# Optimization experiments

Measured on AMD Instinct MI355X. Metric: run time of the kernel, lower is better.

The kernel has to match this reference:

```python
import jax, jax.numpy as jnp
import numpy as np

B, S, D_IN, D_Q, D_V, H = 2, 2048, 1024, 1024, 1024, 16
HD_Q, HD_V = D_Q // H, D_V // H
SCALE = float(D_Q) ** 0.5  # source scales by sqrt(d_q), NOT sqrt(head_dim)


def setup_inputs() -> dict:
    key = jax.random.key(0)
    k1, k2, k3, k4, k5 = jax.random.split(key, 5)
    return {
        "x": jax.random.normal(k1, (B, S, D_IN), dtype=jnp.float32),
        "w_q": jax.random.normal(k2, (D_IN, D_Q), dtype=jnp.float32),
        "w_k": jax.random.normal(k3, (D_IN, D_Q), dtype=jnp.float32),
        "w_v": jax.random.normal(k4, (D_IN, D_V), dtype=jnp.float32),
        "W_o": jax.random.normal(k5, (D_IN, D_V), dtype=jnp.float32),
    }


def reference(x, w_q, w_k, w_v, W_o):
    b, s, _ = x.shape
    # projections: [b, s, d]
    q = x @ w_q
    k = x @ w_k
    v = x @ w_v
    # split heads -> [b, h, s, hd]
    Q = q.reshape(b, s, H, HD_Q).transpose(0, 2, 1, 3)
    K = k.reshape(b, s, H, HD_Q).transpose(0, 2, 1, 3)
    V = v.reshape(b, s, H, HD_V).transpose(0, 2, 1, 3)
    # full [b, h, s, s] score matrix (naive attention, as in source)
    scores = jnp.einsum("bhqd,bhkd->bhqk", Q, K)
    # FAITHFUL QUIRK: source applies softmax over dim=0 (batch axis)
    attn = jax.nn.softmax(scores / SCALE, axis=0)
    vals = jnp.einsum("bhqk,bhkd->bhqd", attn, V)
    vals = vals.transpose(0, 2, 1, 3).reshape(b, s, D_V)
    return vals @ W_o
```

## Files before the change

### kernel.cpp

```cpp
#include <hip/hip_runtime.h>


typedef _Float16 f16;
typedef __attribute__((ext_vector_type(8))) _Float16 f16x8;
typedef __attribute__((ext_vector_type(4))) _Float16 f16x4;
typedef __attribute__((ext_vector_type(4))) float f32x4;
typedef __attribute__((ext_vector_type(16))) float f32x16;

#define MFMA16(a,b,c)  __builtin_amdgcn_mfma_f32_16x16x32_f16(a,b,c,0,0,0)
#define MFMA32(a,b,c)  __builtin_amdgcn_mfma_f32_32x32x16_f16(a,b,c,0,0,0)
#define GLD16(gp, lp) __builtin_amdgcn_global_load_lds(                         \
    (const __attribute__((address_space(1))) void*)(gp),                        \
    (__attribute__((address_space(3))) void*)(lp), 16, 0, 0)

__global__ __launch_bounds__(256) void prep(const float* __restrict__ x,
                                            const float* __restrict__ w0, const float* __restrict__ w1,
                                            const float* __restrict__ w2, const float* __restrict__ w3,
                                            f16* __restrict__ xh,
                                            f16* __restrict__ o0, f16* __restrict__ o1,
                                            f16* __restrict__ o2, f16* __restrict__ o3) {
    const int bb = blockIdx.x;
    const int tid = threadIdx.x;
    if (bb >= 1024) {
        int i = (bb - 1024) * 256 + tid;
        float4 v = ((const float4*)x)[i];
        f16x4 h;
        h[0] = (f16)v.x; h[1] = (f16)v.y; h[2] = (f16)v.z; h[3] = (f16)v.w;
        *(f16x4*)(xh + (long)i * 4) = h;
        return;
    }
    const float* w; f16* o;
    switch (bb & 3) {
        case 0: w = w0; o = o0; break;
        case 1: w = w1; o = o1; break;
        case 2: w = w2; o = o2; break;
        default: w = w3; o = o3; break;
    }
    __shared__ alignas(16) f16 t[64][72];
    const int d0 = ((bb >> 2) & 15) * 64, j0 = (bb >> 6) * 64;
    #pragma unroll
    for (int it = 0; it < 4; ++it) {
        int idx = it * 256 + tid;
        int row = idx >> 4, c4 = idx & 15;
        float4 v = *(const float4*)(w + (long)(d0 + row) * 1024 + j0 + c4 * 4);
        f16x4 h;
        h[0] = (f16)v.x; h[1] = (f16)v.y; h[2] = (f16)v.z; h[3] = (f16)v.w;
        *(f16x4*)&t[row][c4 * 4] = h;
    }
    __syncthreads();
    #pragma unroll
    for (int it = 0; it < 4; ++it) {
        int idx = it * 256 + tid;
        int jr = idx >> 4, d4 = idx & 15;
        f16x4 h;
        #pragma unroll
        for (int m = 0; m < 4; ++m) h[m] = t[d4 * 4 + m][jr];
        *(f16x4*)(o + (long)(j0 + jr) * 1024 + d0 + d4 * 4) = h;
    }
}

__global__ __launch_bounds__(256, 1) void gemm_qkv(const f16* __restrict__ A,
                                                   const f16* __restrict__ Wt,
                                                   f16* __restrict__ Qg,
                                                   f16* __restrict__ Kg,
                                                   f16* __restrict__ Vtg) {
    __shared__ alignas(16) f16 smem[16384];
    f16* As = smem;
    f16* Bs = smem + 8192;
    const int tid = threadIdx.x;
    const int wave = tid >> 6, lane = tid & 63;
    const int l15 = lane & 15, lq = lane >> 4;
    const int sw = l15 & 7;
    const int m0 = blockIdx.x * 128, n0 = blockIdx.y * 128;
    const int wr = (wave >> 1) * 64, wc = (wave & 1) * 64;
    const int r8 = lane >> 3;
    const int swc8 = ((lane & 7) ^ r8) * 8;

    f32x4 acc[4][4] = {};

    for (int kt = 0; kt < 16; ++kt) {
        __syncthreads();
        #pragma unroll
        for (int i = 0; i < 4; ++i) {
            GLD16(A  + (long)(m0 + wave * 32 + i * 8 + r8) * 1024 + kt * 64 + swc8, As + (wave * 32 + i * 8) * 64);
            GLD16(Wt + (long)(n0 + wave * 32 + i * 8 + r8) * 1024 + kt * 64 + swc8, Bs + (wave * 32 + i * 8) * 64);
        }
        __syncthreads();
        #pragma unroll
        for (int s2 = 0; s2 < 2; ++s2) {
            const int rc = ((s2 * 4 + lq) ^ sw) << 3;
            f16x8 af[4], bf[4];
            #pragma unroll
            for (int i = 0; i < 4; ++i) af[i] = *(const f16x8*)&As[(wr + i * 16 + l15) * 64 + rc];
            #pragma unroll
            for (int j = 0; j < 4; ++j) bf[j] = *(const f16x8*)&Bs[(wc + j * 16 + l15) * 64 + rc];
            #pragma unroll
            for (int i = 0; i < 4; ++i)
                #pragma unroll
                for (int j = 0; j < 4; ++j)
                    acc[i][j] = MFMA16(af[i], bf[j], acc[i][j]);
        }
    }

    const int sel = n0 >> 10;
    const int nb = n0 - (sel << 10);

    if (sel < 2) {
        f16* dst = sel == 0 ? Qg : Kg;
        const float qs = sel == 0 ? 0.045084219f : 1.0f;
        __syncthreads();
        #pragma unroll
        for (int i = 0; i < 4; ++i)
            #pragma unroll
            for (int j = 0; j < 4; ++j) {
                int row0 = wr + i * 16 + lq * 4;
                int colb = wc + j * 16 + l15;
                int chunk = colb >> 3, sub = colb & 7;
                #pragma unroll
                for (int r = 0; r < 4; ++r) {
                    int row = row0 + r;
                    smem[row * 128 + ((chunk ^ (row & 7)) << 3) + sub] = (f16)(acc[i][j][r] * qs);
                }
            }
        __syncthreads();
        #pragma unroll
        for (int e = 0; e < 8; ++e) {
            int id = e * 256 + tid;
            int row = id >> 4, c = id & 15;
            f16x8 v = *(const f16x8*)&smem[row * 128 + ((c ^ (row & 7)) << 3)];
            int gr = m0 + row, b = gr >> 11, s = gr & 2047;
            int gc = nb + c * 8, hh = gc >> 6, hd = gc & 63;
            *(f16x8*)(dst + (long)((b * 16 + hh) * 2048 + s) * 64 + hd) = v;
        }
    } else {
        #pragma unroll
        for (int i = 0; i < 4; ++i)
            #pragma unroll
            for (int j = 0; j < 4; ++j) {
                int gr0 = m0 + wr + i * 16 + lq * 4;
                int gc  = nb + wc + j * 16 + l15;
                int b = gr0 >> 11, s = gr0 & 2047;
                int hh = gc >> 6, hd = gc & 63;
                f16x4 v;
                #pragma unroll
                for (int r = 0; r < 4; ++r) v[r] = (f16)acc[i][j][r];
                *(f16x4*)(Vtg + (long)((b * 16 + hh) * 64 + hd) * 2048 + s) = v;
            }
    }
}

template<int NSUM>
__global__ __launch_bounds__(256, 1) void gemm_out(const f16* __restrict__ A0,
                                                   const f16* __restrict__ A1,
                                                   const f16* __restrict__ A2,
                                                   const f16* __restrict__ A3,
                                                   const f16* __restrict__ Bt,
                                                   float* __restrict__ outp) {
    __shared__ alignas(16) f16 As[64][72];
    __shared__ alignas(16) f16 Bs[128][64];
    const int tid = threadIdx.x;
    const int wave = tid >> 6, lane = tid & 63;
    const int l15 = lane & 15, lq = lane >> 4;
    const int sw = l15 & 7;
    const int m0 = blockIdx.x * 64, n0 = blockIdx.y * 128;
    const int wr = (wave >> 1) * 32, wc = (wave & 1) * 64;
    const int r8 = lane >> 3;
    const int swc8 = ((lane & 7) ^ r8) * 8;

    f32x4 acc[2][4] = {};

    for (int kt = 0; kt < 16; ++kt) {
        __syncthreads();
        #pragma unroll
        for (int it = 0; it < 2; ++it) {
            int idx = it * 256 + tid;
            int row = idx >> 3, c = idx & 7;
            long off = (long)(m0 + row) * 1024 + kt * 64 + c * 8;
            f16x8 a = *(const f16x8*)(A0 + off) + *(const f16x8*)(A1 + off);
            if constexpr (NSUM >= 3) a = a + *(const f16x8*)(A2 + off);
            if constexpr (NSUM >= 4) a = a + *(const f16x8*)(A3 + off);
            *(f16x8*)&As[row][c * 8] = a;
        }
        #pragma unroll
        for (int i = 0; i < 4; ++i)
            GLD16(Bt + (long)(n0 + wave * 32 + i * 8 + r8) * 1024 + kt * 64 + swc8, &Bs[wave * 32 + i * 8][0]);
        __syncthreads();
        #pragma unroll
        for (int s2 = 0; s2 < 2; ++s2) {
            const int rc = ((s2 * 4 + lq) ^ sw) << 3;
            f16x8 af[2], bf[4];
            #pragma unroll
            for (int i = 0; i < 2; ++i) af[i] = *(const f16x8*)&As[wr + i * 16 + l15][s2 * 32 + lq * 8];
            #pragma unroll
            for (int j = 0; j < 4; ++j) bf[j] = *(const f16x8*)&Bs[wc + j * 16 + l15][rc];
            #pragma unroll
            for (int i = 0; i < 2; ++i)
                #pragma unroll
                for (int j = 0; j < 4; ++j)
                    acc[i][j] = MFMA16(af[i], bf[j], acc[i][j]);
        }
    }

    #pragma unroll
    for (int i = 0; i < 2; ++i)
        #pragma unroll
        for (int j = 0; j < 4; ++j) {
            int gr0 = m0 + wr + i * 16 + lq * 4;
            int gc  = n0 + wc + j * 16 + l15;
            #pragma unroll
            for (int r = 0; r < 4; ++r)
                outp[(long)(gr0 + r) * 1024 + gc] = acc[i][j][r];
        }
}

__global__ __launch_bounds__(256, 3) void attention_kernel(const f16* __restrict__ Qg,
                                                           const f16* __restrict__ Kg,
                                                           const f16* __restrict__ Vtg,
                                                           f16* __restrict__ v0,
                                                           f16* __restrict__ v1,
                                                           f16* __restrict__ v2) {
    __shared__ alignas(16) f16 Ks [3][2][32][64];
    __shared__ alignas(16) f16 Vts[3][2][64][32];
    const int tid = threadIdx.x;
    const int wave = tid >> 6, lane = tid & 63;
    const int l31 = lane & 31, hi = lane >> 5;
    const int kchunk = l31 & 7;
    const int vcb = (l31 >> 1) & 3;

    const int NS = gridDim.x >> 8;
    const int bid = blockIdx.x;
    const int xcd = bid & 7, sl = bid >> 3;
    const int h  = xcd * 2 + (sl & 1);
    const int qt = (sl >> 1) & 15, ks = sl >> 5;
    const int q0 = qt * 128;
    const int kb = 64 / NS, krem = 64 % NS;
    const int nt = kb + (ks < krem ? 1 : 0);
    const int ts0 = ks * kb + (ks < krem ? ks : krem);
    const int key0 = ts0 * 32;
    f16* vals = ks == 0 ? v0 : ks == 1 ? v1 : v2;
    const int qr = q0 + wave * 32;

    f16x8 qfr[2][4];
    #pragma unroll
    for (int b2 = 0; b2 < 2; ++b2)
        #pragma unroll
        for (int s2 = 0; s2 < 4; ++s2)
            qfr[b2][s2] = *(const f16x8*)(Qg + (long)((b2 * 16 + h) * 2048 + qr + l31) * 64
                                          + s2 * 16 + hi * 8);

    f32x16 acc[2][2] = {};

    const int tb = wave & 1;
    const int r8 = lane >> 3;
    const int swc8 = ((lane & 7) ^ r8) * 8;
    const f16* kbase = Kg  + (long)((tb * 16 + h) * 2048 + key0) * 64 + r8 * 64 + swc8;
    const f16* vbase = Vtg + (long)((tb * 16 + h) * 64 + (lane >> 2)) * 2048 + key0
                       + ((lane & 3) ^ ((lane >> 3) & 3)) * 8;

    auto stage = [&](int kt, int buf) {
        if (wave < 2) {
            const f16* g = kbase + kt * 2048;
            f16* l = &Ks[buf][tb][0][0];
            #pragma unroll
            for (int i = 0; i < 4; ++i) GLD16(g + i * 512, l + i * 512);
        } else {
            const f16* g = vbase + kt * 32;
            f16* l = &Vts[buf][tb][0][0];
            #pragma unroll
            for (int i = 0; i < 4; ++i) GLD16(g + (long)i * 16 * 2048, l + i * 512);
        }
    };

    const f16* VtsF = &Vts[0][0][0][0];
    const f16x8 ones8 = {(f16)1.f,(f16)1.f,(f16)1.f,(f16)1.f,(f16)1.f,(f16)1.f,(f16)1.f,(f16)1.f};

    stage(0, 0);
    stage(1, 1);
    int cur = 0, nx2 = 2;
    for (int kt = 0; kt < nt; ++kt) {
        if (kt == nt - 1) asm volatile("s_waitcnt vmcnt(0)" ::: "memory");
        else              asm volatile("s_waitcnt vmcnt(4)" ::: "memory");
        __builtin_amdgcn_s_barrier();
        __builtin_amdgcn_sched_barrier(0);
        if (kt + 2 < nt) stage(kt + 2, nx2);

        f32x16 S0 = {}, S1 = {};
        __builtin_amdgcn_s_setprio(1);
        #pragma unroll
        for (int s2 = 0; s2 < 4; ++s2) {
            const int rc = ((s2 * 2 + hi) ^ kchunk) << 3;
            f16x8 a0 = *(const f16x8*)&Ks[cur][0][l31][rc];
            f16x8 a1 = *(const f16x8*)&Ks[cur][1][l31][rc];
            S0 = MFMA32(a0, qfr[0][s2], S0);
            S1 = MFMA32(a1, qfr[1][s2], S1);
        }
        __builtin_amdgcn_s_setprio(0);

        unsigned pk[8];
        #pragma unroll
        for (int p = 0; p < 8; ++p) {
            float e0 = __builtin_amdgcn_exp2f(S1[2 * p]     - S0[2 * p]);
            float e1 = __builtin_amdgcn_exp2f(S1[2 * p + 1] - S0[2 * p + 1]);
            float pa = __builtin_amdgcn_rcpf(1.0f + e0);
            float pb = __builtin_amdgcn_rcpf(1.0f + e1);
            auto h2 = __builtin_amdgcn_cvt_pkrtz(pa, pb);
            pk[p] = __builtin_bit_cast(unsigned, h2);
        }

        f16x8 pf0[2], pf1[2];
        #pragma unroll
        for (int keyh = 0; keyh < 2; ++keyh) {
            unsigned a0 = pk[4 * keyh + 0], b0 = pk[4 * keyh + 2];
            unsigned a1 = pk[4 * keyh + 1], b1 = pk[4 * keyh + 3];
            asm("v_permlane32_swap_b32 %0, %1" : "+v"(a0), "+v"(b0));
            asm("v_permlane32_swap_b32 %0, %1" : "+v"(a1), "+v"(b1));
            union { unsigned u[4]; f16x8 v; } m;
            m.u[0] = a0; m.u[1] = a1; m.u[2] = b0; m.u[3] = b1;
            pf0[keyh] = m.v;
            pf1[keyh] = ones8 - m.v;
        }

        __builtin_amdgcn_s_setprio(1);
        #pragma unroll
        for (int pb = 0; pb < 2; ++pb)
            #pragma unroll
            for (int keyh = 0; keyh < 2; ++keyh) {
                const f16x8 pfr = pb ? pf1[keyh] : pf0[keyh];
                #pragma unroll
                for (int hdh = 0; hdh < 2; ++hdh) {
                    f16x8 vf = *(const f16x8*)&VtsF[cur * 4096 + pb * 2048 + hdh * 1024
                                                    + l31 * 32 + (((keyh * 2 + hi) ^ vcb) << 3)];
                    acc[pb][hdh] = MFMA32(vf, pfr, acc[pb][hdh]);
                }
            }
        __builtin_amdgcn_s_setprio(0);

        cur = cur == 2 ? 0 : cur + 1;
        nx2 = nx2 == 2 ? 0 : nx2 + 1;
    }

    #pragma unroll
    for (int pb = 0; pb < 2; ++pb)
        #pragma unroll
        for (int hdh = 0; hdh < 2; ++hdh)
            #pragma unroll
            for (int g = 0; g < 4; ++g) {
                f16x4 ov;
                #pragma unroll
                for (int r2 = 0; r2 < 4; ++r2) ov[r2] = (f16)acc[pb][hdh][g * 4 + r2];
                *(f16x4*)(vals + (long)(pb * 2048 + qr + l31) * 1024
                          + h * 64 + hdh * 32 + g * 8 + hi * 4) = ov;
            }
}

extern "C" void kernel_launch(void* const* d_in, const int* in_sizes, int n_in,
                              void* d_out, int out_size, void* d_ws, size_t ws_size,
                              hipStream_t stream) {
    const float* x  = (const float*)d_in[0];
    const float* wq = (const float*)d_in[1];
    const float* wk = (const float*)d_in[2];
    const float* wv = (const float*)d_in[3];
    const float* wo = (const float*)d_in[4];

    char* ws = (char*)d_ws;
    f16* xh    = (f16*)(ws);
    f16* wqT   = (f16*)(ws + 8388608);
    f16* wkT   = (f16*)(ws + 10485760);
    f16* wvT   = (f16*)(ws + 12582912);
    f16* woT   = (f16*)(ws + 14680064);
    f16* Qg    = (f16*)(ws + 16777216);
    f16* Kg    = (f16*)(ws + 25165824);
    f16* Vtg   = (f16*)(ws + 33554432);
    f16* vals1 = (f16*)(ws + 41943040);
    f16* vals2 = (f16*)(ws + 50331648);
    f16* vals0 = xh;
    (void)in_sizes; (void)n_in; (void)out_size;

    const int NS = (ws_size >= (size_t)58720256) ? 3 : 2;

    prep<<<5120, 256, 0, stream>>>(x, wq, wk, wv, wo, xh, wqT, wkT, wvT, woT);

    gemm_qkv<<<dim3(32, 24), 256, 0, stream>>>(xh, wqT, Qg, Kg, Vtg);

    attention_kernel<<<NS * 256, 256, 0, stream>>>(Qg, Kg, Vtg, vals0, vals1, vals2);

    if (NS == 3)
        gemm_out<3><<<dim3(64, 8), 256, 0, stream>>>(vals0, vals1, vals2, vals0, woT, (float*)d_out);
    else
        gemm_out<2><<<dim3(64, 8), 256, 0, stream>>>(vals0, vals1, vals0, vals0, woT, (float*)d_out);
}
```

Before: 192.9 us.

## Fold batch-difference scores into one 128-wide dot and widen per-wave query tiles

The QKV GEMM now writes Q and K for both batches side by side as 128-wide rows, with batch-0 K negated. A single 128-deep score MFMA chain then yields S1-S0 directly, replacing the two separate 64-deep chains and the subtraction. The attention kernel gives each wave 64 queries in two groups so each V fragment loaded from LDS feeds twice as many MFMAs. It also fixes the key split at 4 ways of 512 keys, adds a fourth partial-output buffer, and lowers the occupancy hint to 2. In exchange it needs more registers and a larger workspace, and the old guard on workspace size is gone.

```diff
diff --git a/kernel.cpp b/kernel.cpp
--- a/kernel.cpp
+++ b/kernel.cpp
@@ -61,8 +61,8 @@
 
 __global__ __launch_bounds__(256, 1) void gemm_qkv(const f16* __restrict__ A,
                                                    const f16* __restrict__ Wt,
-                                                   f16* __restrict__ Qg,
-                                                   f16* __restrict__ Kg,
+                                                   f16* __restrict__ Qc,
+                                                   f16* __restrict__ Kc,
                                                    f16* __restrict__ Vtg) {
     __shared__ alignas(16) f16 smem[16384];
     f16* As = smem;
@@ -106,8 +106,11 @@
     const int nb = n0 - (sel << 10);
 
     if (sel < 2) {
-        f16* dst = sel == 0 ? Qg : Kg;
-        const float qs = sel == 0 ? 0.045084219f : 1.0f;
+        f16* dst = sel == 0 ? Qc : Kc;
+        const int b = m0 >> 11;
+        const int boff = b ? 0 : 64;
+        const float qs = sel == 0 ? 0.045084219f
+                                  : (b == 0 ? -1.0f : 1.0f);
         __syncthreads();
         #pragma unroll
         for (int i = 0; i < 4; ++i)
@@ -128,9 +131,9 @@
             int id = e * 256 + tid;
             int row = id >> 4, c = id & 15;
             f16x8 v = *(const f16x8*)&smem[row * 128 + ((c ^ (row & 7)) << 3)];
-            int gr = m0 + row, b = gr >> 11, s = gr & 2047;
+            int gr = m0 + row, s = gr & 2047;
             int gc = nb + c * 8, hh = gc >> 6, hd = gc & 63;
-            *(f16x8*)(dst + (long)((b * 16 + hh) * 2048 + s) * 64 + hd) = v;
+            *(f16x8*)(dst + (long)(hh * 2048 + s) * 128 + boff + hd) = v;
         }
     } else {
         #pragma unroll
@@ -213,56 +216,55 @@
         }
 }
 
-__global__ __launch_bounds__(256, 3) void attention_kernel(const f16* __restrict__ Qg,
-                                                           const f16* __restrict__ Kg,
+__global__ __launch_bounds__(256, 2) void attention_kernel(const f16* __restrict__ Qc,
+                                                           const f16* __restrict__ Kc,
                                                            const f16* __restrict__ Vtg,
                                                            f16* __restrict__ v0,
                                                            f16* __restrict__ v1,
-                                                           f16* __restrict__ v2) {
-    __shared__ alignas(16) f16 Ks [3][2][32][64];
+                                                           f16* __restrict__ v2,
+                                                           f16* __restrict__ v3) {
+    __shared__ alignas(16) f16 KsC[3][32][128];
     __shared__ alignas(16) f16 Vts[3][2][64][32];
     const int tid = threadIdx.x;
     const int wave = tid >> 6, lane = tid & 63;
     const int l31 = lane & 31, hi = lane >> 5;
-    const int kchunk = l31 & 7;
+    const int kch = l31 & 15;
     const int vcb = (l31 >> 1) & 3;
 
-    const int NS = gridDim.x >> 8;
     const int bid = blockIdx.x;
     const int xcd = bid & 7, sl = bid >> 3;
     const int h  = xcd * 2 + (sl & 1);
-    const int qt = (sl >> 1) & 15, ks = sl >> 5;
-    const int q0 = qt * 128;
-    const int kb = 64 / NS, krem = 64 % NS;
-    const int nt = kb + (ks < krem ? 1 : 0);
-    const int ts0 = ks * kb + (ks < krem ? ks : krem);
-    const int key0 = ts0 * 32;
-    f16* vals = ks == 0 ? v0 : ks == 1 ? v1 : v2;
-    const int qr = q0 + wave * 32;
-
-    f16x8 qfr[2][4];
-    #pragma unroll
-    for (int b2 = 0; b2 < 2; ++b2)
-        #pragma unroll
-        for (int s2 = 0; s2 < 4; ++s2)
-            qfr[b2][s2] = *(const f16x8*)(Qg + (long)((b2 * 16 + h) * 2048 + qr + l31) * 64
-                                          + s2 * 16 + hi * 8);
-
-    f32x16 acc[2][2] = {};
-
+    const int qt = (sl >> 1) & 7, ks = sl >> 4;
+    const int q0 = qt * 256;
+    const int key0 = ks * 512;
+    const int nt = 16;
+    f16* vals = ks == 0 ? v0 : ks == 1 ? v1 : ks == 2 ? v2 : v3;
+    const int qr = q0 + wave * 64;
+
+    f16x8 qfr[2][8];
+    #pragma unroll
+    for (int g = 0; g < 2; ++g)
+        #pragma unroll
+        for (int s2 = 0; s2 < 8; ++s2)
+            qfr[g][s2] = *(const f16x8*)(Qc + (long)(h * 2048 + qr + g * 32 + l31) * 128
+                                         + s2 * 16 + hi * 8);
+
+    f32x16 acc[2][2][2] = {};
+
+    const int kw = wave & 1;
+    const f16* kbase = Kc + (long)(h * 2048 + key0 + kw * 16 + (lane >> 4)) * 128;
     const int tb = wave & 1;
-    const int r8 = lane >> 3;
-    const int swc8 = ((lane & 7) ^ r8) * 8;
-    const f16* kbase = Kg  + (long)((tb * 16 + h) * 2048 + key0) * 64 + r8 * 64 + swc8;
     const f16* vbase = Vtg + (long)((tb * 16 + h) * 64 + (lane >> 2)) * 2048 + key0
                        + ((lane & 3) ^ ((lane >> 3) & 3)) * 8;
 
     auto stage = [&](int kt, int buf) {
         if (wave < 2) {
-            const f16* g = kbase + kt * 2048;
-            f16* l = &Ks[buf][tb][0][0];
-            #pragma unroll
-            for (int i = 0; i < 4; ++i) GLD16(g + i * 512, l + i * 512);
+            f16* l = &KsC[buf][0][0] + kw * 2048;
+            #pragma unroll
+            for (int i = 0; i < 4; ++i) {
+                const int gch = ((lane & 15) ^ ((i << 2) | (lane >> 4))) << 3;
+                GLD16(kbase + (long)kt * 4096 + i * 512 + gch, l + i * 512);
+            }
         } else {
             const f16* g = vbase + kt * 32;
             f16* l = &Vts[buf][tb][0][0];
@@ -284,53 +286,56 @@
         __builtin_amdgcn_sched_barrier(0);
         if (kt + 2 < nt) stage(kt + 2, nx2);
 
-        f32x16 S0 = {}, S1 = {};
+        f16x8 pf0[2][2];
+        #pragma unroll
+        for (int g = 0; g < 2; ++g) {
+            f32x16 S = {};
+            __builtin_amdgcn_s_setprio(1);
+            #pragma unroll
+            for (int s2 = 0; s2 < 8; ++s2) {
+                f16x8 a = *(const f16x8*)&KsC[cur][l31][(((s2 * 2 + hi) ^ kch) << 3)];
+                S = MFMA32(a, qfr[g][s2], S);
+            }
+            __builtin_amdgcn_s_setprio(0);
+
+            unsigned pk[8];
+            #pragma unroll
+            for (int p = 0; p < 8; ++p) {
+                float e0 = __builtin_amdgcn_exp2f(S[2 * p]);
+                float e1 = __builtin_amdgcn_exp2f(S[2 * p + 1]);
+                float pa = __builtin_amdgcn_rcpf(1.0f + e0);
+                float pb = __builtin_amdgcn_rcpf(1.0f + e1);
+                auto h2 = __builtin_amdgcn_cvt_pkrtz(pa, pb);
+                pk[p] = __builtin_bit_cast(unsigned, h2);
+            }
+            #pragma unroll
+            for (int keyh = 0; keyh < 2; ++keyh) {
+                unsigned a0 = pk[4 * keyh + 0], b0 = pk[4 * keyh + 2];
+                unsigned a1 = pk[4 * keyh + 1], b1 = pk[4 * keyh + 3];
+                asm("v_permlane32_swap_b32 %0, %1" : "+v"(a0), "+v"(b0));
+                asm("v_permlane32_swap_b32 %0, %1" : "+v"(a1), "+v"(b1));
+                union { unsigned u[4]; f16x8 v; } m;
+                m.u[0] = a0; m.u[1] = a1; m.u[2] = b0; m.u[3] = b1;
+                pf0[g][keyh] = m.v;
+            }
+        }
+
         __builtin_amdgcn_s_setprio(1);
         #pragma unroll
-        for (int s2 = 0; s2 < 4; ++s2) {
-            const int rc = ((s2 * 2 + hi) ^ kchunk) << 3;
-            f16x8 a0 = *(const f16x8*)&Ks[cur][0][l31][rc];
-            f16x8 a1 = *(const f16x8*)&Ks[cur][1][l31][rc];
-            S0 = MFMA32(a0, qfr[0][s2], S0);
-            S1 = MFMA32(a1, qfr[1][s2], S1);
-        }
-        __builtin_amdgcn_s_setprio(0);
-
-        unsigned pk[8];
-        #pragma unroll
-        for (int p = 0; p < 8; ++p) {
-            float e0 = __builtin_amdgcn_exp2f(S1[2 * p]     - S0[2 * p]);
-            float e1 = __builtin_amdgcn_exp2f(S1[2 * p + 1] - S0[2 * p + 1]);
-            float pa = __builtin_amdgcn_rcpf(1.0f + e0);
-            float pb = __builtin_amdgcn_rcpf(1.0f + e1);
-            auto h2 = __builtin_amdgcn_cvt_pkrtz(pa, pb);
-            pk[p] = __builtin_bit_cast(unsigned, h2);
-        }
-
-        f16x8 pf0[2], pf1[2];
-        #pragma unroll
-        for (int keyh = 0; keyh < 2; ++keyh) {
-            unsigned a0 = pk[4 * keyh + 0], b0 = pk[4 * keyh + 2];
-            unsigned a1 = pk[4 * keyh + 1], b1 = pk[4 * keyh + 3];
-            asm("v_permlane32_swap_b32 %0, %1" : "+v"(a0), "+v"(b0));
-            asm("v_permlane32_swap_b32 %0, %1" : "+v"(a1), "+v"(b1));
-            union { unsigned u[4]; f16x8 v; } m;
-            m.u[0] = a0; m.u[1] = a1; m.u[2] = b0; m.u[3] = b1;
-            pf0[keyh] = m.v;
-            pf1[keyh] = ones8 - m.v;
-        }
-
-        __builtin_amdgcn_s_setprio(1);
-        #pragma unroll
         for (int pb = 0; pb < 2; ++pb)
             #pragma unroll
             for (int keyh = 0; keyh < 2; ++keyh) {
-                const f16x8 pfr = pb ? pf1[keyh] : pf0[keyh];
-                #pragma unroll
-                for (int hdh = 0; hdh < 2; ++hdh) {
-                    f16x8 vf = *(const f16x8*)&VtsF[cur * 4096 + pb * 2048 + hdh * 1024
-                                                    + l31 * 32 + (((keyh * 2 + hi) ^ vcb) << 3)];
-                    acc[pb][hdh] = MFMA32(vf, pfr, acc[pb][hdh]);
+                f16x8 vf[2];
+                #pragma unroll
+                for (int hdh = 0; hdh < 2; ++hdh)
+                    vf[hdh] = *(const f16x8*)&VtsF[cur * 4096 + pb * 2048 + hdh * 1024
+                                                   + l31 * 32 + (((keyh * 2 + hi) ^ vcb) << 3)];
+                #pragma unroll
+                for (int g = 0; g < 2; ++g) {
+                    const f16x8 pfr = pb ? (ones8 - pf0[g][keyh]) : pf0[g][keyh];
+                    #pragma unroll
+                    for (int hdh = 0; hdh < 2; ++hdh)
+                        acc[pb][g][hdh] = MFMA32(vf[hdh], pfr, acc[pb][g][hdh]);
                 }
             }
         __builtin_amdgcn_s_setprio(0);
@@ -342,15 +347,17 @@
     #pragma unroll
     for (int pb = 0; pb < 2; ++pb)
         #pragma unroll
-        for (int hdh = 0; hdh < 2; ++hdh)
-            #pragma unroll
-            for (int g = 0; g < 4; ++g) {
-                f16x4 ov;
-                #pragma unroll
-                for (int r2 = 0; r2 < 4; ++r2) ov[r2] = (f16)acc[pb][hdh][g * 4 + r2];
-                *(f16x4*)(vals + (long)(pb * 2048 + qr + l31) * 1024
-                          + h * 64 + hdh * 32 + g * 8 + hi * 4) = ov;
-            }
+        for (int g = 0; g < 2; ++g)
+            #pragma unroll
+            for (int hdh = 0; hdh < 2; ++hdh)
+                #pragma unroll
+                for (int gg = 0; gg < 4; ++gg) {
+                    f16x4 ov;
+                    #pragma unroll
+                    for (int r2 = 0; r2 < 4; ++r2) ov[r2] = (f16)acc[pb][g][hdh][gg * 4 + r2];
+                    *(f16x4*)(vals + (long)(pb * 2048 + qr + g * 32 + l31) * 1024
+                              + h * 64 + hdh * 32 + gg * 8 + hi * 4) = ov;
+                }
 }
 
 extern "C" void kernel_launch(void* const* d_in, const int* in_sizes, int n_in,
@@ -368,24 +375,20 @@
     f16* wkT   = (f16*)(ws + 10485760);
     f16* wvT   = (f16*)(ws + 12582912);
     f16* woT   = (f16*)(ws + 14680064);
-    f16* Qg    = (f16*)(ws + 16777216);
-    f16* Kg    = (f16*)(ws + 25165824);
+    f16* Qc    = (f16*)(ws + 16777216);
+    f16* Kc    = (f16*)(ws + 25165824);
     f16* Vtg   = (f16*)(ws + 33554432);
     f16* vals1 = (f16*)(ws + 41943040);
     f16* vals2 = (f16*)(ws + 50331648);
+    f16* vals3 = (f16*)(ws + 58720256);
     f16* vals0 = xh;
-    (void)in_sizes; (void)n_in; (void)out_size;
-
-    const int NS = (ws_size >= (size_t)58720256) ? 3 : 2;
+    (void)in_sizes; (void)n_in; (void)out_size; (void)ws_size;
 
     prep<<<5120, 256, 0, stream>>>(x, wq, wk, wv, wo, xh, wqT, wkT, wvT, woT);
 
-    gemm_qkv<<<dim3(32, 24), 256, 0, stream>>>(xh, wqT, Qg, Kg, Vtg);
-
-    attention_kernel<<<NS * 256, 256, 0, stream>>>(Qg, Kg, Vtg, vals0, vals1, vals2);
-
-    if (NS == 3)
-        gemm_out<3><<<dim3(64, 8), 256, 0, stream>>>(vals0, vals1, vals2, vals0, woT, (float*)d_out);
-    else
-        gemm_out<2><<<dim3(64, 8), 256, 0, stream>>>(vals0, vals1, vals0, vals0, woT, (float*)d_out);
-}
+    gemm_qkv<<<dim3(32, 24), 256, 0, stream>>>(xh, wqT, Qc, Kc, Vtg);
+
+    attention_kernel<<<512, 256, 0, stream>>>(Qc, Kc, Vtg, vals0, vals1, vals2, vals3);
+
+    gemm_out<4><<<dim3(64, 8), 256, 0, stream>>>(vals0, vals1, vals2, vals3, woT, (float*)d_out);
+}
```

Result: no change. 191.3 us (-0.8%).
